# Kernel tuning notes

Measured on AMD Instinct MI355X. Metric: run time of the kernel, lower is better.

Reference implementation:

```python
import math
import jax, jax.numpy as jnp
import numpy as np

B, N, C_IN, C_OUT = 16, 1024, 256, 256


def setup_inputs() -> dict:
    key = jax.random.key(0)
    k_x, k_q, k_k, k_v, k_s, k_e = jax.random.split(key, 6)
    x = jax.random.normal(k_x, (B, N, C_IN), dtype=jnp.float32)
    # torch Linear(in, out, bias=False) == x @ W with W: [in, out]
    sc = 1.0 / math.sqrt(C_IN)
    W_q = jax.random.normal(k_q, (C_IN, C_OUT), dtype=jnp.float32) * sc
    W_k = jax.random.normal(k_k, (C_IN, C_OUT), dtype=jnp.float32) * sc
    W_v = jax.random.normal(k_v, (C_IN, C_OUT), dtype=jnp.float32) * sc
    W_sigma = jax.random.normal(k_s, (C_IN, 1), dtype=jnp.float32) * sc
    # fixed standard-normal noise replacing torch.normal's on-the-fly sampling
    eps = jax.random.normal(k_e, (B, N, N), dtype=jnp.float32)
    return {"x": x, "W_q": W_q, "W_k": W_k, "W_v": W_v,
            "W_sigma": W_sigma, "eps": eps}


def reference(x, W_q, W_k, W_v, W_sigma, eps):
    n = x.shape[1]
    d_model = W_q.shape[1]
    Q = x @ W_q            # [B, n, d]
    K = x @ W_k            # [B, n, d]
    V = x @ W_v            # [B, n, d]
    sigma = x @ W_sigma    # [B, n, 1]

    # prior association: gaussian = Normal(mean=|i-j|, std=|sigma|), row-normalized
    idx = jnp.arange(n)
    p = jnp.abs(idx[:, None] - idx[None, :]).astype(x.dtype)   # [n, n]
    gaussian = p[None, :, :] + jnp.abs(sigma) * eps            # [B, n, n]
    P = gaussian / jnp.sum(gaussian, axis=-1, keepdims=True)

    # series association: softmax over dim=0 (batch), exactly as the torch code
    scores = jnp.einsum('bnd,bmd->bnm', Q, K) / math.sqrt(d_model)
    S = jax.nn.softmax(scores, axis=0)

    Z = jnp.einsum('bnm,bmd->bnd', S, V)                       # reconstruction
    return Z, P, S
```

## Files before the change

kernel.cpp:

```cpp
#include <hip/hip_runtime.h>
#include <hip/hip_bf16.h>
#include <math.h>

#define B_ 16
#define N_ 1024
#define C_ 256

typedef unsigned short ushort_t;
typedef __attribute__((ext_vector_type(8))) short short8;
typedef __attribute__((ext_vector_type(4))) float f32x4;

static __device__ __forceinline__ ushort_t f2bf(float f) {
    __hip_bfloat16 h = __float2bfloat16(f);
    return *(ushort_t*)&h;
}

static __device__ __forceinline__ float bf2f(ushort_t u) {
    return __uint_as_float(((unsigned int)u) << 16);
}

static __device__ __forceinline__ void async16(const ushort_t* g, ushort_t* l) {
    __builtin_amdgcn_global_load_lds(
        (const __attribute__((address_space(1))) unsigned int*)g,
        (__attribute__((address_space(3))) unsigned int*)l,
        16, 0, 0);
}

static __device__ __forceinline__ void xcd_swz(int lid, int nwg, int gx, int gy,
                                               int& bx, int& by, int& bz)
{
    const int cpx = nwg >> 3;
    const int s = (lid & 7) * cpx + (lid >> 3);
    bx = s % gx;
    const int t = s / gx;
    by = t % gy;
    bz = t / gy;
}

template <int OUT_BF16, int NT>
static __device__ __forceinline__ void gemm_body(
    int bx, int by, int bz, ushort_t* sh,
    const ushort_t* __restrict__ A, const ushort_t* __restrict__ B,
    void* __restrict__ Cp, int N, int K, long sA, long sB, long sC, float alpha)
{
    A += (long)bz * sA;
    B += (long)bz * sB;

    const int LDSZ = (128 + NT) * 32;
    float* shF = (float*)sh;

    const int tid  = threadIdx.x;
    const int wave = tid >> 6;
    const int lane = tid & 63;
    const int wm   = wave >> 2;
    const int wn   = wave & 3;
    const int WC   = NT >> 2;
    const int row0 = by * 128;
    const int col0 = bx * NT;

    const int r_grp = lane >> 2;
    const int c_chk = lane & 3;
    const int swz   = c_chk ^ ((r_grp >> 1) & 3);

    const ushort_t* agp = A + (long)(row0 + wave * 16 + r_grp) * K + swz * 8;
    const ushort_t* bgp = B + (long)(col0 + wave * 16 + r_grp) * K + swz * 8;
    const bool stB = (NT == 128) || (wave < (NT >> 4));

    const int lr16 = lane & 15;
    const int q16  = lane >> 4;
    const int slot = (q16 ^ ((lr16 >> 1) & 3)) * 8;

    f32x4 acc[4][NT / 64] = {};

    {
        ushort_t* As = sh;
        ushort_t* Bs = sh + 128 * 32;
        async16(agp, &As[wave * 512]);
        if (stB) async16(bgp, &Bs[wave * 512]);
    }
    __syncthreads();

    int p = 0;
    for (int k0 = 0; k0 < K; k0 += 32) {
        if (k0 + 32 < K) {
            ushort_t* As = sh + (p ^ 1) * LDSZ;
            ushort_t* Bs = As + 128 * 32;
            async16(agp + k0 + 32, &As[wave * 512]);
            if (stB) async16(bgp + k0 + 32, &Bs[wave * 512]);
        }

        const ushort_t* As = sh + p * LDSZ;
        const ushort_t* Bs = As + 128 * 32;
        short8 av[4], bv[NT / 64];
#pragma unroll
        for (int i = 0; i < 4; i++)
            av[i] = *(const short8*)&As[(wm * 64 + i * 16 + lr16) * 32 + slot];
#pragma unroll
        for (int j = 0; j < NT / 64; j++)
            bv[j] = *(const short8*)&Bs[(wn * WC + j * 16 + lr16) * 32 + slot];

#pragma unroll
        for (int i = 0; i < 4; i++)
#pragma unroll
            for (int j = 0; j < NT / 64; j++)
                acc[i][j] = __builtin_amdgcn_mfma_f32_16x16x32_bf16(
                    av[i], bv[j], acc[i][j], 0, 0, 0);

        __syncthreads();
        p ^= 1;
    }

#pragma unroll
    for (int i = 0; i < 4; i++) {
#pragma unroll
        for (int j = 0; j < NT / 64; j++) {
            const int rl = wm * 16 + q16 * 4;
            const int cl = wn * WC + j * 16 + lr16;
#pragma unroll
            for (int r = 0; r < 4; r++) {
                const int rr = rl + r;
                const int xr = ((rr >> 2) & 1) << 4;
                shF[rr * NT + (cl ^ xr)] = alpha * acc[i][j][r];
            }
        }
        __syncthreads();

        if constexpr (OUT_BF16) {
            ushort_t* C = (ushort_t*)Cp + (long)bz * sC;
            const int idx = tid;
            const int rl = idx >> 4;
            const int c8 = idx & 15;
            const int xr4 = ((rl >> 2) & 1) << 2;
            const int gr = row0 + (rl >> 4) * 64 + i * 16 + (rl & 15);
            const float4 a = ((const float4*)(shF + rl * 128))[(c8 * 2) ^ xr4];
            const float4 b = ((const float4*)(shF + rl * 128))[(c8 * 2 + 1) ^ xr4];
            short8 pk;
            pk[0] = (short)f2bf(a.x); pk[1] = (short)f2bf(a.y);
            pk[2] = (short)f2bf(a.z); pk[3] = (short)f2bf(a.w);
            pk[4] = (short)f2bf(b.x); pk[5] = (short)f2bf(b.y);
            pk[6] = (short)f2bf(b.z); pk[7] = (short)f2bf(b.w);
            *(short8*)(C + (long)gr * N + col0 + c8 * 8) = pk;
        } else {
            float* C = (float*)Cp + (long)bz * sC;
#pragma unroll
            for (int v = 0; v < NT / 64; v++) {
                const int idx = v * 512 + tid;
                const int rl = idx / (NT / 4);
                const int c4 = idx & (NT / 4 - 1);
                const int xr4 = ((rl >> 2) & 1) << 2;
                const int gr = row0 + (rl >> 4) * 64 + i * 16 + (rl & 15);
                const float4 val = ((const float4*)(shF + rl * NT))[c4 ^ xr4];
                *(float4*)(C + (long)gr * N + col0 + c4 * 4) = val;
            }
        }
        __syncthreads();
    }
}

template <int OUT_BF16, int NT>
__global__ __launch_bounds__(512) void gemm_nt(
    const ushort_t* __restrict__ A, const ushort_t* __restrict__ B,
    void* __restrict__ Cp, int N, int K, long sA, long sB, long sC, float alpha)
{
    __shared__ ushort_t sh[2 * (128 + NT) * 32];
    const int gx = gridDim.x, gy = gridDim.y;
    const int nwg = gx * gy * (int)gridDim.z;
    int bx, by, bz;
    xcd_swz(blockIdx.x + gx * (blockIdx.y + gy * (int)blockIdx.z), nwg, gx, gy,
            bx, by, bz);
    gemm_body<OUT_BF16, NT>(bx, by, bz, sh, A, B, Cp, N, K, sA, sB, sC, alpha);
}

__global__ __launch_bounds__(512) void scores_tr_fused(
    const ushort_t* __restrict__ Q, const ushort_t* __restrict__ Kb,
    ushort_t* __restrict__ Sc, const ushort_t* __restrict__ V,
    ushort_t* __restrict__ VT)
{
    __shared__ ushort_t sh[2 * 256 * 32];
    const int id = blockIdx.x;
    if (id < 1024) {
        int bx, by, bz;
        xcd_swz(id, 1024, 8, 8, bx, by, bz);
        gemm_body<1, 128>(bx, by, bz, sh, Q, Kb, Sc, N_, C_,
                          (long)N_ * C_, (long)N_ * C_, (long)N_ * N_, 0.0625f);
    } else {
        const int b2  = id - 1024;
        const int bz  = b2 >> 7;
        const int rem = b2 & 127;
        const int sub = threadIdx.x >> 8;
        const int n0  = (rem & 7) * 32;
        const int m0  = ((rem >> 3) * 2 + sub) * 32;
        const int tix = threadIdx.x & 255;
        const int tx = tix & 31, ty = tix >> 5;
        ushort_t (*t2)[32][33] = (ushort_t (*)[32][33])sh;
        const long NC = (long)N_ * C_;
        const ushort_t* Vb = V + (long)bz * NC;
        ushort_t* Tb = VT + (long)bz * NC;
#pragma unroll
        for (int j = 0; j < 4; j++)
            t2[sub][ty + j * 8][tx] = Vb[(long)(m0 + ty + j * 8) * C_ + n0 + tx];
        __syncthreads();
#pragma unroll
        for (int j = 0; j < 4; j++)
            Tb[(long)(n0 + ty + j * 8) * N_ + m0 + tx] = t2[sub][tx][ty + j * 8];
    }
}

__global__ __launch_bounds__(256) void cast_fused(
    const float* __restrict__ x, ushort_t* __restrict__ xbf,
    const float* __restrict__ Wq, const float* __restrict__ Wk,
    const float* __restrict__ Wv, ushort_t* __restrict__ WbfT,
    const float* __restrict__ Wsig, float* __restrict__ asig)
{
    __shared__ float t[32][33];
    const int blk = blockIdx.x;
    if (blk < 4096) {
        const long i = ((long)blk * 256 + threadIdx.x) * 4;
        const float4 v = *(const float4*)(x + i);
        ushort4 o;
        o.x = f2bf(v.x); o.y = f2bf(v.y); o.z = f2bf(v.z); o.w = f2bf(v.w);
        *(ushort4*)(xbf + i) = o;
        if (asig) {
            const int lane = threadIdx.x & 63;
            const float4 w = *(const float4*)(Wsig + lane * 4);
            float d = v.x * w.x + v.y * w.y + v.z * w.z + v.w * w.w;
#pragma unroll
            for (int off = 32; off; off >>= 1) d += __shfl_down(d, off, 64);
            if (lane == 0) asig[blk * 4 + (threadIdx.x >> 6)] = fabsf(d);
        }
    } else {
        const int m = blk - 4096;
        const float* W = ((m >> 6) == 0) ? Wq : ((m >> 6) == 1) ? Wk : Wv;
        const int rem = m & 63;
        const int n0 = (rem & 7) * 32, k0 = (rem >> 3) * 32;
        const int tx = threadIdx.x & 31, ty = threadIdx.x >> 5;
#pragma unroll
        for (int j = 0; j < 4; j++)
            t[ty + j * 8][tx] = W[(long)(k0 + ty + j * 8) * 256 + n0 + tx];
        __syncthreads();
        ushort_t* o = WbfT + (long)(m >> 6) * 65536;
#pragma unroll
        for (int j = 0; j < 4; j++)
            o[(long)(n0 + ty + j * 8) * 256 + k0 + tx] = f2bf(t[tx][ty + j * 8]);
    }
}

__global__ __launch_bounds__(256) void softmax_batch(
    ushort_t* __restrict__ Sc, float* __restrict__ S)
{
    const long NN = (long)N_ * N_;
    const long i4 = ((long)blockIdx.x * 256 + threadIdx.x) * 4;

    float4 v[B_];
    float sx = 0.f, sy = 0.f, sz = 0.f, sw = 0.f;
#pragma unroll
    for (int b = 0; b < B_; b++) {
        const ushort4 u = *(const ushort4*)(Sc + (long)b * NN + i4);
        v[b].x = __expf(bf2f(u.x)); sx += v[b].x;
        v[b].y = __expf(bf2f(u.y)); sy += v[b].y;
        v[b].z = __expf(bf2f(u.z)); sz += v[b].z;
        v[b].w = __expf(bf2f(u.w)); sw += v[b].w;
    }
    const float ix = 1.0f / sx, iy = 1.0f / sy, iz = 1.0f / sz, iw = 1.0f / sw;
#pragma unroll
    for (int b = 0; b < B_; b++) {
        float4 o;
        o.x = v[b].x * ix; o.y = v[b].y * iy;
        o.z = v[b].z * iz; o.w = v[b].w * iw;
        *(float4*)(S + (long)b * NN + i4) = o;
        ushort4 ob;
        ob.x = f2bf(o.x); ob.y = f2bf(o.y); ob.z = f2bf(o.z); ob.w = f2bf(o.w);
        *(ushort4*)(Sc + (long)b * NN + i4) = ob;
    }
}

__global__ __launch_bounds__(256) void p_kernel(
    const float* __restrict__ x, const float* __restrict__ Wsig,
    const float* __restrict__ eps, float* __restrict__ P,
    const float* __restrict__ asig)
{
    const int row  = blockIdx.x * 4 + (threadIdx.x >> 6);
    const int lane = threadIdx.x & 63;
    const int n = row & (N_ - 1);

    float a;
    if (asig) {
        a = asig[row];
    } else {
        const float4 xv = *(const float4*)(x + (long)row * C_ + lane * 4);
        const float4 wv = *(const float4*)(Wsig + lane * 4);
        float d = xv.x * wv.x + xv.y * wv.y + xv.z * wv.z + xv.w * wv.w;
#pragma unroll
        for (int off = 32; off; off >>= 1) d += __shfl_xor(d, off, 64);
        a = fabsf(d);
    }

    const float4* erow = (const float4*)(eps + (long)row * N_);
    float4 g[4];
    float sum = 0.f;
#pragma unroll
    for (int k = 0; k < 4; k++) {
        const float4 e = erow[k * 64 + lane];
        const int j0 = (k * 64 + lane) * 4;
        g[k].x = (float)abs(n - (j0 + 0)) + a * e.x;
        g[k].y = (float)abs(n - (j0 + 1)) + a * e.y;
        g[k].z = (float)abs(n - (j0 + 2)) + a * e.z;
        g[k].w = (float)abs(n - (j0 + 3)) + a * e.w;
        sum += g[k].x + g[k].y + g[k].z + g[k].w;
    }
#pragma unroll
    for (int off = 32; off; off >>= 1) sum += __shfl_xor(sum, off, 64);
    const float inv = 1.0f / sum;

    float4* prow = (float4*)(P + (long)row * N_);
#pragma unroll
    for (int k = 0; k < 4; k++) {
        float4 o;
        o.x = g[k].x * inv; o.y = g[k].y * inv;
        o.z = g[k].z * inv; o.w = g[k].w * inv;
        prow[k * 64 + lane] = o;
    }
}

extern "C" void kernel_launch(void* const* d_in, const int* in_sizes, int n_in,
                              void* d_out, int out_size, void* d_ws, size_t ws_size,
                              hipStream_t stream)
{
    const float* x    = (const float*)d_in[0];
    const float* Wq   = (const float*)d_in[1];
    const float* Wk   = (const float*)d_in[2];
    const float* Wv   = (const float*)d_in[3];
    const float* Wsig = (const float*)d_in[4];
    const float* eps  = (const float*)d_in[5];
    float* out = (float*)d_out;

    const long ZN = (long)B_ * N_ * C_;
    const long PN = (long)B_ * N_ * N_;
    const long NC = (long)N_ * C_;
    const long NN = (long)N_ * N_;

    float* Zp = out;
    float* Pp = out + ZN;
    float* Sp = out + ZN + PN;

    ushort_t* base = (ushort_t*)Pp;
    ushort_t* Qbf  = base;
    ushort_t* Kbf  = base + ZN;
    ushort_t* Vbf  = base + 2 * ZN;
    ushort_t* xbf  = base + 3 * ZN;
    ushort_t* VbfT = base + 3 * ZN;
    ushort_t* WbfT = base + 4 * ZN;
    ushort_t* Scbf = base + 4 * ZN;

    float* asig = (d_ws && ws_size >= (size_t)(B_ * N_) * sizeof(float))
                      ? (float*)d_ws : nullptr;

    const dim3 blk(256);
    const dim3 blk512(512);

    cast_fused<<<dim3(4096 + 192), blk, 0, stream>>>(
        x, xbf, Wq, Wk, Wv, WbfT, Wsig, asig);

    gemm_nt<1, 128><<<dim3(2, 128, 3), blk512, 0, stream>>>(
        xbf, WbfT, Qbf, C_, C_, 0, 65536, ZN, 1.0f);

    scores_tr_fused<<<dim3(1024 + 2048), blk512, 0, stream>>>(
        Qbf, Kbf, Scbf, Vbf, VbfT);

    softmax_batch<<<dim3(NN / 1024), blk, 0, stream>>>(Scbf, Sp);

    gemm_nt<0, 64><<<dim3(4, 8, 16), blk512, 0, stream>>>(
        Scbf, VbfT, Zp, C_, N_, NN, NC, NC, 1.0f);

    p_kernel<<<dim3((B_ * N_) / 4), blk, 0, stream>>>(
        x, Wsig, eps, Pp, asig);
}
```

Baseline: 274.3 us.

## Fuse Z GEMM and P normalization into one launch using workspace buffers

```diff
diff --git a/kernel.cpp b/kernel.cpp
--- a/kernel.cpp
+++ b/kernel.cpp
@@ -171,6 +171,39 @@
     gemm_body<OUT_BF16, NT>(bx, by, bz, sh, A, B, Cp, N, K, sA, sB, sC, alpha);
 }
 
+static __device__ __forceinline__ void p_row(
+    int row, float a, const float* __restrict__ eps, float* __restrict__ P)
+{
+    const int lane = threadIdx.x & 63;
+    const int n = row & (N_ - 1);
+
+    const float4* erow = (const float4*)(eps + (long)row * N_);
+    float4 g[4];
+    float sum = 0.f;
+#pragma unroll
+    for (int k = 0; k < 4; k++) {
+        const float4 e = erow[k * 64 + lane];
+        const int j0 = (k * 64 + lane) * 4;
+        g[k].x = (float)abs(n - (j0 + 0)) + a * e.x;
+        g[k].y = (float)abs(n - (j0 + 1)) + a * e.y;
+        g[k].z = (float)abs(n - (j0 + 2)) + a * e.z;
+        g[k].w = (float)abs(n - (j0 + 3)) + a * e.w;
+        sum += g[k].x + g[k].y + g[k].z + g[k].w;
+    }
+#pragma unroll
+    for (int off = 32; off; off >>= 1) sum += __shfl_xor(sum, off, 64);
+    const float inv = 1.0f / sum;
+
+    float4* prow = (float4*)(P + (long)row * N_);
+#pragma unroll
+    for (int k = 0; k < 4; k++) {
+        float4 o;
+        o.x = g[k].x * inv; o.y = g[k].y * inv;
+        o.z = g[k].z * inv; o.w = g[k].w * inv;
+        prow[k * 64 + lane] = o;
+    }
+}
+
 __global__ __launch_bounds__(512) void scores_tr_fused(
     const ushort_t* __restrict__ Q, const ushort_t* __restrict__ Kb,
     ushort_t* __restrict__ Sc, const ushort_t* __restrict__ V,
@@ -206,6 +239,24 @@
     }
 }
 
+__global__ __launch_bounds__(512) void zp_fused(
+    const ushort_t* __restrict__ Sc, const ushort_t* __restrict__ VT,
+    float* __restrict__ Z, const float* __restrict__ eps,
+    float* __restrict__ P, const float* __restrict__ asig)
+{
+    __shared__ ushort_t sh[2 * (128 + 64) * 32];
+    const int id = blockIdx.x;
+    if (id < 512) {
+        int bx, by, bz;
+        xcd_swz(id, 512, 4, 8, bx, by, bz);
+        gemm_body<0, 64>(bx, by, bz, sh, Sc, VT, Z, C_, N_,
+                         (long)N_ * N_, (long)N_ * C_, (long)N_ * C_, 1.0f);
+    } else {
+        const int row = (id - 512) * 8 + (threadIdx.x >> 6);
+        p_row(row, asig[row], eps, P);
+    }
+}
+
 __global__ __launch_bounds__(256) void cast_fused(
     const float* __restrict__ x, ushort_t* __restrict__ xbf,
     const float* __restrict__ Wq, const float* __restrict__ Wk,
@@ -281,7 +332,6 @@
 {
     const int row  = blockIdx.x * 4 + (threadIdx.x >> 6);
     const int lane = threadIdx.x & 63;
-    const int n = row & (N_ - 1);
 
     float a;
     if (asig) {
@@ -294,32 +344,7 @@
         for (int off = 32; off; off >>= 1) d += __shfl_xor(d, off, 64);
         a = fabsf(d);
     }
-
-    const float4* erow = (const float4*)(eps + (long)row * N_);
-    float4 g[4];
-    float sum = 0.f;
-#pragma unroll
-    for (int k = 0; k < 4; k++) {
-        const float4 e = erow[k * 64 + lane];
-        const int j0 = (k * 64 + lane) * 4;
-        g[k].x = (float)abs(n - (j0 + 0)) + a * e.x;
-        g[k].y = (float)abs(n - (j0 + 1)) + a * e.y;
-        g[k].z = (float)abs(n - (j0 + 2)) + a * e.z;
-        g[k].w = (float)abs(n - (j0 + 3)) + a * e.w;
-        sum += g[k].x + g[k].y + g[k].z + g[k].w;
-    }
-#pragma unroll
-    for (int off = 32; off; off >>= 1) sum += __shfl_xor(sum, off, 64);
-    const float inv = 1.0f / sum;
-
-    float4* prow = (float4*)(P + (long)row * N_);
-#pragma unroll
-    for (int k = 0; k < 4; k++) {
-        float4 o;
-        o.x = g[k].x * inv; o.y = g[k].y * inv;
-        o.z = g[k].z * inv; o.w = g[k].w * inv;
-        prow[k * 64 + lane] = o;
-    }
+    p_row(row, a, eps, P);
 }
 
 extern "C" void kernel_launch(void* const* d_in, const int* in_sizes, int n_in,
@@ -348,12 +373,23 @@
     ushort_t* Kbf  = base + ZN;
     ushort_t* Vbf  = base + 2 * ZN;
     ushort_t* xbf  = base + 3 * ZN;
-    ushort_t* VbfT = base + 3 * ZN;
     ushort_t* WbfT = base + 4 * ZN;
-    ushort_t* Scbf = base + 4 * ZN;
-
-    float* asig = (d_ws && ws_size >= (size_t)(B_ * N_) * sizeof(float))
-                      ? (float*)d_ws : nullptr;
+
+    const size_t need = (size_t)65536 + (size_t)(ZN + PN) * 2;
+    const bool big_ws = (d_ws != nullptr) && (ws_size >= need);
+
+    float* asig;
+    ushort_t *VbfT, *Scbf;
+    if (big_ws) {
+        asig = (float*)d_ws;
+        VbfT = (ushort_t*)d_ws + 32768;
+        Scbf = VbfT + ZN;
+    } else {
+        asig = (d_ws && ws_size >= (size_t)(B_ * N_) * sizeof(float))
+                   ? (float*)d_ws : nullptr;
+        VbfT = base + 3 * ZN;
+        Scbf = base + 4 * ZN;
+    }
 
     const dim3 blk(256);
     const dim3 blk512(512);
@@ -369,9 +405,13 @@
 
     softmax_batch<<<dim3(NN / 1024), blk, 0, stream>>>(Scbf, Sp);
 
-    gemm_nt<0, 64><<<dim3(4, 8, 16), blk512, 0, stream>>>(
-        Scbf, VbfT, Zp, C_, N_, NN, NC, NC, 1.0f);
-
-    p_kernel<<<dim3((B_ * N_) / 4), blk, 0, stream>>>(
-        x, Wsig, eps, Pp, asig);
-}
+    if (big_ws) {
+        zp_fused<<<dim3(512 + 2048), blk512, 0, stream>>>(
+            Scbf, VbfT, Zp, eps, Pp, asig);
+    } else {
+        gemm_nt<0, 64><<<dim3(4, 8, 16), blk512, 0, stream>>>(
+            Scbf, VbfT, Zp, C_, N_, NN, NC, NC, 1.0f);
+        p_kernel<<<dim3((B_ * N_) / 4), blk, 0, stream>>>(
+            x, Wsig, eps, Pp, asig);
+    }
+}
```

New measurement: 272.3 us. No clear change (-0.7%).
